# Optimization experiments

Hardware: AMD Instinct MI355X
Metric: run time of the kernel (lower is better)

Reference implementation:

```python
import jax, jax.numpy as jnp
import numpy as np

N_NODES = 10000
N_MOTIFS = 2500          # N_NODES / subgraph_size(=4)
N_AUG = N_NODES + N_MOTIFS
N_EDGES = 500000
NFEAT = 512
NHID = 128


def setup_inputs() -> dict:
    key = jax.random.key(0)
    ks = jax.random.split(key, 14)
    s = 0.05  # param init scale
    return {
        "x": jax.random.normal(ks[0], (N_NODES, NFEAT), jnp.float32),
        "edge_index": jax.random.randint(ks[1], (2, N_EDGES), 0, N_AUG, jnp.int64),
        "motif_list": jax.random.randint(ks[2], (N_MOTIFS, 4), 0, N_NODES, jnp.int64),
        "W1": jax.random.normal(ks[3], (NFEAT, 2 * NHID), jnp.float32) * s,
        "a_src1": jax.random.normal(ks[4], (2 * NHID,), jnp.float32) * s,
        "a_dst1": jax.random.normal(ks[5], (2 * NHID,), jnp.float32) * s,
        "b1": jnp.zeros((2 * NHID,), jnp.float32),
        "W2": jax.random.normal(ks[6], (2 * NHID, NHID), jnp.float32) * s,
        "a_src2": jax.random.normal(ks[7], (NHID,), jnp.float32) * s,
        "a_dst2": jax.random.normal(ks[8], (NHID,), jnp.float32) * s,
        "b2": jnp.zeros((NHID,), jnp.float32),
        "W_lin": jax.random.normal(ks[9], (NFEAT, NHID), jnp.float32) * s,  # torch Linear(nhid, nfeat) weight
        "b_lin": jnp.zeros((NFEAT,), jnp.float32),
    }


def gat_layer(x, src, dst, W, a_s, a_d, b, n):
    """Single-head GATConv (PyG semantics): edge-softmax attention over dst."""
    h = x @ W                                              # [n, out]
    alpha_s = h @ a_s                                      # [n]
    alpha_d = h @ a_d                                      # [n]
    e = jax.nn.leaky_relu(alpha_s[src] + alpha_d[dst], 0.2)  # [E]
    m = jax.ops.segment_max(e, dst, num_segments=n)        # stable softmax per dst
    w = jnp.exp(e - m[dst])
    denom = jax.ops.segment_sum(w, dst, num_segments=n)
    coef = w / (denom[dst] + 1e-16)                        # [E]
    out = jax.ops.segment_sum(coef[:, None] * h[src], dst, num_segments=n)
    return out + b


def reference(x, edge_index, motif_list, W1, a_src1, a_dst1, b1,
              W2, a_src2, a_dst2, b2, W_lin, b_lin):
    n = x.shape[0] + motif_list.shape[0]
    # augmented features: mean of each motif's node features appended as motif nodes
    x_aug = jnp.concatenate([x, jnp.mean(x[motif_list], axis=1)], axis=0)  # [N_AUG, F]
    # augmented edge list + self loops (GATConv adds self loops)
    loops = jnp.arange(n, dtype=edge_index.dtype)
    src = jnp.concatenate([edge_index[0], loops])
    dst = jnp.concatenate([edge_index[1], loops])
    h1 = gat_layer(x_aug, src, dst, W1, a_src1, a_dst1, b1, n)   # [N_AUG, 2*NHID]
    h2 = gat_layer(h1, src, dst, W2, a_src2, a_dst2, b2, n)      # [N_AUG, NHID]
    rec_adj = jax.nn.sigmoid(h2 @ h2.T)                          # [N_AUG, N_AUG]
    rec_feature = jax.nn.sigmoid(h2 @ W_lin.T + b_lin)           # [N_AUG, NFEAT]
    return (rec_feature, rec_adj)
```

## Files before the change

kernel.cpp:

```cpp
#include <hip/hip_runtime.h>

typedef unsigned short u16;
typedef unsigned int   u32;
typedef __attribute__((ext_vector_type(8))) short short8;
typedef __attribute__((ext_vector_type(4))) float f32x4;

#define N_NODES 10000
#define N_MOTIFS 2500
#define N_AUG   12500
#define N_EDGES 500000
#define E_TOT   512500
#define NFEAT   512
#define NH1     256
#define NH2     128

__device__ __forceinline__ float b2f(u16 u){ return __uint_as_float(((u32)u) << 16); }
__device__ __forceinline__ u16 f2b(float f){
  u32 x = __float_as_uint(f);
  x += 0x7fffu + ((x >> 16) & 1u);
  return (u16)(x >> 16);
}

#define PREP_Z   (N_AUG + 8)
#define PREP_W1  (NFEAT * NH1)
#define PREP_W2  (NH1 * NH2)
#define PREP_WL  (NFEAT * NH2)
#define PREP_TOT (PREP_Z + PREP_W1 + PREP_W2 + PREP_WL)

__global__ void k_prep(const float* __restrict__ W1, const float* __restrict__ W2,
                       const float* __restrict__ Wl, int* __restrict__ cnt,
                       u16* __restrict__ W1T, u16* __restrict__ W2T, u16* __restrict__ Wlb){
  int i = blockIdx.x * blockDim.x + threadIdx.x;
  if (i < PREP_Z){ cnt[i] = 0; return; }
  i -= PREP_Z;
  if (i < PREP_W1){
    int r = i / NH1, c = i - r * NH1;
    W1T[(size_t)c * NFEAT + r] = f2b(W1[i]);
    return;
  }
  i -= PREP_W1;
  if (i < PREP_W2){
    int r = i / NH2, c = i - r * NH2;
    W2T[(size_t)c * NH1 + r] = f2b(W2[i]);
    return;
  }
  i -= PREP_W2;
  if (i < PREP_WL) Wlb[i] = f2b(Wl[i]);
}

__global__ void k_xaug(const float* __restrict__ x, const int* __restrict__ motif,
                       u16* __restrict__ xb){
  int gid = blockIdx.x * blockDim.x + threadIdx.x;
  int row = gid >> 6;
  int c   = (gid & 63) << 3;
  if (row >= N_AUG) return;
  float v[8];
  if (row < N_NODES){
    const float* s = &x[(size_t)row * NFEAT + c];
    #pragma unroll
    for (int k = 0; k < 8; ++k) v[k] = s[k];
  } else {
    int m = row - N_NODES;
    const float* p0 = &x[(size_t)motif[m*4+0] * NFEAT + c];
    const float* p1 = &x[(size_t)motif[m*4+1] * NFEAT + c];
    const float* p2 = &x[(size_t)motif[m*4+2] * NFEAT + c];
    const float* p3 = &x[(size_t)motif[m*4+3] * NFEAT + c];
    #pragma unroll
    for (int k = 0; k < 8; ++k) v[k] = (p0[k] + p1[k] + p2[k] + p3[k]) * 0.25f;
  }
  short8 o;
  #pragma unroll
  for (int k = 0; k < 8; ++k) o[k] = (short)f2b(v[k]);
  *(short8*)&xb[(size_t)row * NFEAT + c] = o;
}

__global__ void k_hist(const int* __restrict__ ei, int* __restrict__ cnt){
  int i = blockIdx.x * blockDim.x + threadIdx.x;
  if (i >= E_TOT) return;
  int d = (i < N_EDGES) ? ei[N_EDGES + i] : (i - N_EDGES);
  atomicAdd(&cnt[d], 1);
}

__global__ void k_scan(const int* __restrict__ cnt, int* __restrict__ offs, int* __restrict__ cur){
  __shared__ int part[1024];
  int t = threadIdx.x;
  const int CH = 13;
  int base = t * CH;
  int s = 0;
  for (int i = 0; i < CH; ++i){ int idx = base + i; if (idx < N_AUG) s += cnt[idx]; }
  part[t] = s;
  __syncthreads();
  for (int off = 1; off < 1024; off <<= 1){
    int v = 0;
    if (t >= off) v = part[t - off];
    __syncthreads();
    if (t >= off) part[t] += v;
    __syncthreads();
  }
  int run = (t == 0) ? 0 : part[t - 1];
  for (int i = 0; i < CH; ++i){
    int idx = base + i;
    if (idx <= N_AUG){
      offs[idx] = run;
      if (idx < N_AUG){ cur[idx] = run; run += cnt[idx]; }
    }
  }
}

__global__ void k_scatter(const int* __restrict__ ei, int* __restrict__ cur, int* __restrict__ srcs){
  int i = blockIdx.x * blockDim.x + threadIdx.x;
  if (i >= E_TOT) return;
  int s, d;
  if (i < N_EDGES){ s = ei[i]; d = ei[N_EDGES + i]; } else { s = i - N_EDGES; d = s; }
  int pos = atomicAdd(&cur[d], 1);
  srcs[pos] = s;
}

template<int DIM>
__global__ void k_alpha(const u16* __restrict__ h, const float* __restrict__ avs,
                        const float* __restrict__ avd, float* __restrict__ oS, float* __restrict__ oD){
  __shared__ float shS[8], shD[8];
  int n = blockIdx.x, t = threadIdx.x;
  int lane = t & 63, wid = t >> 6;
  float hv = b2f(h[(size_t)n * DIM + t]);
  float s = hv * avs[t];
  float d = hv * avd[t];
  #pragma unroll
  for (int o = 32; o; o >>= 1){ s += __shfl_down(s, o); d += __shfl_down(d, o); }
  if (lane == 0){ shS[wid] = s; shD[wid] = d; }
  __syncthreads();
  if (t == 0){
    float ss = 0.f, dd = 0.f;
    #pragma unroll
    for (int i = 0; i < DIM/64; ++i){ ss += shS[i]; dd += shD[i]; }
    oS[n] = ss; oD[n] = dd;
  }
}

template<int DIM, int T>
__global__ __launch_bounds__(T) void k_agg(
    const int* __restrict__ offs, const int* __restrict__ srcs,
    const float* __restrict__ aS, const float* __restrict__ aD,
    const u16* __restrict__ hb, const float* __restrict__ bias,
    u16* __restrict__ hout){
  constexpr int NW = T / 64;
  __shared__ float rsh[2];
  __shared__ float wsh[128];
  __shared__ int   ssh[128];
  int d = blockIdx.x, t = threadIdx.x;
  int lane = t & 63, wid = t >> 6;
  int r0 = offs[d], r1 = offs[d + 1];
  float adv = aD[d];

  float mx = -3.0e38f;
  for (int j = r0 + t; j < r1; j += T){
    float e = aS[srcs[j]] + adv;
    e = (e >= 0.f) ? e : 0.2f * e;
    mx = fmaxf(mx, e);
  }
  #pragma unroll
  for (int o = 32; o; o >>= 1) mx = fmaxf(mx, __shfl_down(mx, o));
  if constexpr (NW == 2){
    if (lane == 0) rsh[wid] = mx;
    __syncthreads();
    mx = fmaxf(rsh[0], rsh[1]);
    __syncthreads();
  } else {
    mx = __shfl(mx, 0);
  }

  float sm = 0.f;
  for (int j = r0 + t; j < r1; j += T){
    float e = aS[srcs[j]] + adv;
    e = (e >= 0.f) ? e : 0.2f * e;
    sm += __expf(e - mx);
  }
  #pragma unroll
  for (int o = 32; o; o >>= 1) sm += __shfl_down(sm, o);
  if constexpr (NW == 2){
    if (lane == 0) rsh[wid] = sm;
    __syncthreads();
    sm = rsh[0] + rsh[1];
  } else {
    sm = __shfl(sm, 0);
  }

  float a0 = 0.f, a1 = 0.f;
  for (int base = r0; base < r1; base += 128){
    int cntE = min(128, r1 - base);
    __syncthreads();
    for (int j = t; j < cntE; j += T){
      int s = srcs[base + j];
      ssh[j] = s;
      float e = aS[s] + adv;
      e = (e >= 0.f) ? e : 0.2f * e;
      wsh[j] = __expf(e - mx);
    }
    __syncthreads();
    #pragma unroll 4
    for (int j = 0; j < cntE; ++j){
      u32 v = *(const u32*)&hb[(size_t)ssh[j] * DIM + 2*t];
      float w = wsh[j];
      a0 = fmaf(w, b2f((u16)(v & 0xffffu)), a0);
      a1 = fmaf(w, b2f((u16)(v >> 16)), a1);
    }
  }
  float inv = 1.f / (sm + 1e-16f);
  float o0 = a0 * inv + bias[2*t];
  float o1 = a1 * inv + bias[2*t + 1];
  u32 pv = (u32)f2b(o0) | ((u32)f2b(o1) << 16);
  *(u32*)&hout[(size_t)d * DIM + 2*t] = pv;
}

template<int EPI>
__global__ __launch_bounds__(256) void k_gemm(
    const u16* __restrict__ A, const u16* __restrict__ B,
    void* __restrict__ Cv, const float* __restrict__ bias,
    int M, int N, int K){
  __shared__ union SM {
    struct { u16 As[128][72]; u16 Bs[128][72]; } ab;
    float stage[64][132];
  } sm;
  int t = threadIdx.x;
  int lane = t & 63, wid = t >> 6;
  int wm = wid >> 1, wn = wid & 1;
  int m0 = blockIdx.y * 128, n0 = blockIdx.x * 128;

  f32x4 acc[4][4];
  #pragma unroll
  for (int i = 0; i < 4; ++i)
    #pragma unroll
    for (int j = 0; j < 4; ++j)
      acc[i][j] = {0.f, 0.f, 0.f, 0.f};

  for (int k0 = 0; k0 < K; k0 += 64){
    __syncthreads();
    #pragma unroll
    for (int i = 0; i < 4; ++i){
      int id = t + i * 256;
      int r = id >> 3, c = (id & 7) << 3;
      int gm = m0 + r; if (gm >= M) gm = M - 1;
      int gn = n0 + r; if (gn >= N) gn = N - 1;
      *(short8*)&sm.ab.As[r][c] = *(const short8*)&A[(size_t)gm * K + k0 + c];
      *(short8*)&sm.ab.Bs[r][c] = *(const short8*)&B[(size_t)gn * K + k0 + c];
    }
    __syncthreads();
    #pragma unroll
    for (int kk = 0; kk < 2; ++kk){
      int kof = kk * 32 + (lane >> 4) * 8;
      short8 af[4], bfr[4];
      #pragma unroll
      for (int mi = 0; mi < 4; ++mi) af[mi]  = *(const short8*)&sm.ab.As[wm*64 + mi*16 + (lane & 15)][kof];
      #pragma unroll
      for (int ni = 0; ni < 4; ++ni) bfr[ni] = *(const short8*)&sm.ab.Bs[wn*64 + ni*16 + (lane & 15)][kof];
      #pragma unroll
      for (int mi = 0; mi < 4; ++mi)
        #pragma unroll
        for (int ni = 0; ni < 4; ++ni)
          acc[mi][ni] = __builtin_amdgcn_mfma_f32_16x16x32_bf16(af[mi], bfr[ni], acc[mi][ni], 0, 0, 0);
    }
  }

  if (EPI == 0){
    u16* C = (u16*)Cv;
    #pragma unroll
    for (int mi = 0; mi < 4; ++mi)
      #pragma unroll
      for (int ni = 0; ni < 4; ++ni){
        int gn = n0 + wn*64 + ni*16 + (lane & 15);
        if (gn >= N) continue;
        #pragma unroll
        for (int r = 0; r < 4; ++r){
          int gm = m0 + wm*64 + mi*16 + (lane >> 4)*4 + r;
          if (gm >= M) continue;
          C[(size_t)gm * N + gn] = f2b(acc[mi][ni][r]);
        }
      }
  } else {
    float* C = (float*)Cv;
    #pragma unroll
    for (int half = 0; half < 2; ++half){
      __syncthreads();
      if (wm == half){
        #pragma unroll
        for (int mi = 0; mi < 4; ++mi)
          #pragma unroll
          for (int ni = 0; ni < 4; ++ni){
            int col = wn*64 + ni*16 + (lane & 15);
            int gn  = n0 + col;
            int gnc = (gn < N) ? gn : (N - 1);
            #pragma unroll
            for (int r = 0; r < 4; ++r){
              int lrow = mi*16 + (lane >> 4)*4 + r;
              float v = acc[mi][ni][r];
              if (EPI == 2) v += bias[gnc];
              v = 1.f / (1.f + __expf(-v));
              sm.stage[lrow][col] = v;
            }
          }
      }
      __syncthreads();
      #pragma unroll
      for (int pss = 0; pss < 8; ++pss){
        int flat = pss * 1024 + t * 4;
        int lr = flat >> 7, c = flat & 127;
        int gm = m0 + half*64 + lr;
        if (gm >= M) continue;
        int gn = n0 + c;
        f32x4 v = *(const f32x4*)&sm.stage[lr][c];
        if (gn + 3 < N){
          __builtin_nontemporal_store(v, (f32x4*)&C[(size_t)gm * N + gn]);
        } else {
          #pragma unroll
          for (int e = 0; e < 4; ++e)
            if (gn + e < N) C[(size_t)gm * N + gn + e] = v[e];
        }
      }
    }
  }
}

extern "C" void kernel_launch(void* const* d_in, const int* in_sizes, int n_in,
                              void* d_out, int out_size, void* d_ws, size_t ws_size,
                              hipStream_t stream){
  const float* x    = (const float*)d_in[0];
  const int*   ei   = (const int*)d_in[1];
  const int*   mot  = (const int*)d_in[2];
  const float* W1   = (const float*)d_in[3];
  const float* a_s1 = (const float*)d_in[4];
  const float* a_d1 = (const float*)d_in[5];
  const float* b1   = (const float*)d_in[6];
  const float* W2   = (const float*)d_in[7];
  const float* a_s2 = (const float*)d_in[8];
  const float* a_d2 = (const float*)d_in[9];
  const float* b2   = (const float*)d_in[10];
  const float* Wl   = (const float*)d_in[11];
  const float* bl   = (const float*)d_in[12];

  char* p = (char*)d_ws;
  auto alloc = [&](size_t bytes){ void* r = (void*)p; p += (bytes + 255) & ~(size_t)255; return r; };
  u16*   xaugb = (u16*)alloc((size_t)N_AUG * NFEAT * 2);
  u16*   W1T   = (u16*)alloc((size_t)NH1 * NFEAT * 2);
  u16*   W2T   = (u16*)alloc((size_t)NH2 * NH1 * 2);
  u16*   Wlb   = (u16*)alloc((size_t)NFEAT * NH2 * 2);
  u16*   h1b   = (u16*)alloc((size_t)N_AUG * NH1 * 2);
  u16*   h1out = (u16*)alloc((size_t)N_AUG * NH1 * 2);
  u16*   h2b   = (u16*)alloc((size_t)N_AUG * NH2 * 2);
  u16*   h2o   = (u16*)alloc((size_t)N_AUG * NH2 * 2);
  float* aS    = (float*)alloc((size_t)N_AUG * 4);
  float* aD    = (float*)alloc((size_t)N_AUG * 4);
  int*   cnt   = (int*)alloc((size_t)(N_AUG + 8) * 4);
  int*   offs  = (int*)alloc((size_t)(N_AUG + 8) * 4);
  int*   cur   = (int*)alloc((size_t)(N_AUG + 8) * 4);
  int*   srcs  = (int*)alloc((size_t)E_TOT * 4);

  float* out_feat = (float*)d_out;
  float* out_adj  = out_feat + (size_t)N_AUG * NFEAT;

  k_prep<<<(PREP_TOT + 255) / 256, 256, 0, stream>>>(W1, W2, Wl, cnt, W1T, W2T, Wlb);
  k_xaug<<<(N_AUG * 64 + 255) / 256, 256, 0, stream>>>(x, mot, xaugb);
  k_hist<<<(E_TOT + 255) / 256, 256, 0, stream>>>(ei, cnt);
  k_scan<<<1, 1024, 0, stream>>>(cnt, offs, cur);
  k_scatter<<<(E_TOT + 255) / 256, 256, 0, stream>>>(ei, cur, srcs);

  { dim3 g(NH1 / 128, 98); k_gemm<0><<<g, 256, 0, stream>>>(xaugb, W1T, h1b, nullptr, N_AUG, NH1, NFEAT); }
  k_alpha<NH1><<<N_AUG, NH1, 0, stream>>>(h1b, a_s1, a_d1, aS, aD);
  k_agg<NH1, 128><<<N_AUG, 128, 0, stream>>>(offs, srcs, aS, aD, h1b, b1, h1out);

  { dim3 g(1, 98); k_gemm<0><<<g, 256, 0, stream>>>(h1out, W2T, h2b, nullptr, N_AUG, NH2, NH1); }
  k_alpha<NH2><<<N_AUG, NH2, 0, stream>>>(h2b, a_s2, a_d2, aS, aD);
  k_agg<NH2, 64><<<N_AUG, 64, 0, stream>>>(offs, srcs, aS, aD, h2b, b2, h2o);

  { dim3 g(NFEAT / 128, 98); k_gemm<2><<<g, 256, 0, stream>>>(h2o, Wlb, out_feat, bl, N_AUG, NFEAT, NH2); }
  { dim3 g(98, 98);          k_gemm<1><<<g, 256, 0, stream>>>(h2o, h2o, out_adj, nullptr, N_AUG, N_AUG, NH2); }
}
```

Baseline: 434.0 us.

## Reassociate layer-1 aggregation with W2 and drop softmax max pass

Uses linearity to multiply h1 by W2 before the layer-1 edge aggregation, so the aggregation gathers 128-wide rows instead of 256-wide ones. The bias term becomes b1·W2, precomputed in the prep kernel. The aggregation kernel also drops the separate max and sum passes and computes unnormalized exp weights and their sum in a single pass. This removes two gather passes over edges but risks overflow in exp without max subtraction, and adds extra bf16 rounding from the reordered products.

```diff
diff --git a/kernel.cpp b/kernel.cpp
--- a/kernel.cpp
+++ b/kernel.cpp
@@ -25,11 +25,14 @@
 #define PREP_W1  (NFEAT * NH1)
 #define PREP_W2  (NH1 * NH2)
 #define PREP_WL  (NFEAT * NH2)
-#define PREP_TOT (PREP_Z + PREP_W1 + PREP_W2 + PREP_WL)
+#define PREP_B   (NH2)
+#define PREP_TOT (PREP_Z + PREP_W1 + PREP_W2 + PREP_WL + PREP_B)
 
 __global__ void k_prep(const float* __restrict__ W1, const float* __restrict__ W2,
-                       const float* __restrict__ Wl, int* __restrict__ cnt,
-                       u16* __restrict__ W1T, u16* __restrict__ W2T, u16* __restrict__ Wlb){
+                       const float* __restrict__ Wl, const float* __restrict__ b1,
+                       int* __restrict__ cnt,
+                       u16* __restrict__ W1T, u16* __restrict__ W2T, u16* __restrict__ Wlb,
+                       float* __restrict__ b1W2){
   int i = blockIdx.x * blockDim.x + threadIdx.x;
   if (i < PREP_Z){ cnt[i] = 0; return; }
   i -= PREP_Z;
@@ -45,7 +48,14 @@
     return;
   }
   i -= PREP_W2;
-  if (i < PREP_WL) Wlb[i] = f2b(Wl[i]);
+  if (i < PREP_WL){ Wlb[i] = f2b(Wl[i]); return; }
+  i -= PREP_WL;
+  if (i < PREP_B){
+    float s = 0.f;
+    #pragma unroll 8
+    for (int k = 0; k < NH1; ++k) s += b1[k] * W2[(size_t)k * NH2 + i];
+    b1W2[i] = s;
+  }
 }
 
 __global__ void k_xaug(const float* __restrict__ x, const int* __restrict__ motif,
@@ -137,79 +147,47 @@
   }
 }
 
-template<int DIM, int T>
-__global__ __launch_bounds__(T) void k_agg(
+__global__ __launch_bounds__(64) void k_agg128(
     const int* __restrict__ offs, const int* __restrict__ srcs,
     const float* __restrict__ aS, const float* __restrict__ aD,
     const u16* __restrict__ hb, const float* __restrict__ bias,
     u16* __restrict__ hout){
-  constexpr int NW = T / 64;
-  __shared__ float rsh[2];
   __shared__ float wsh[128];
   __shared__ int   ssh[128];
   int d = blockIdx.x, t = threadIdx.x;
-  int lane = t & 63, wid = t >> 6;
   int r0 = offs[d], r1 = offs[d + 1];
   float adv = aD[d];
 
-  float mx = -3.0e38f;
-  for (int j = r0 + t; j < r1; j += T){
-    float e = aS[srcs[j]] + adv;
-    e = (e >= 0.f) ? e : 0.2f * e;
-    mx = fmaxf(mx, e);
-  }
-  #pragma unroll
-  for (int o = 32; o; o >>= 1) mx = fmaxf(mx, __shfl_down(mx, o));
-  if constexpr (NW == 2){
-    if (lane == 0) rsh[wid] = mx;
-    __syncthreads();
-    mx = fmaxf(rsh[0], rsh[1]);
-    __syncthreads();
-  } else {
-    mx = __shfl(mx, 0);
-  }
-
-  float sm = 0.f;
-  for (int j = r0 + t; j < r1; j += T){
-    float e = aS[srcs[j]] + adv;
-    e = (e >= 0.f) ? e : 0.2f * e;
-    sm += __expf(e - mx);
-  }
-  #pragma unroll
-  for (int o = 32; o; o >>= 1) sm += __shfl_down(sm, o);
-  if constexpr (NW == 2){
-    if (lane == 0) rsh[wid] = sm;
-    __syncthreads();
-    sm = rsh[0] + rsh[1];
-  } else {
-    sm = __shfl(sm, 0);
-  }
-
-  float a0 = 0.f, a1 = 0.f;
+  float a0 = 0.f, a1 = 0.f, smp = 0.f;
   for (int base = r0; base < r1; base += 128){
     int cntE = min(128, r1 - base);
     __syncthreads();
-    for (int j = t; j < cntE; j += T){
+    for (int j = t; j < cntE; j += 64){
       int s = srcs[base + j];
       ssh[j] = s;
       float e = aS[s] + adv;
       e = (e >= 0.f) ? e : 0.2f * e;
-      wsh[j] = __expf(e - mx);
+      float w = __expf(e);
+      wsh[j] = w;
+      smp += w;
     }
     __syncthreads();
     #pragma unroll 4
     for (int j = 0; j < cntE; ++j){
-      u32 v = *(const u32*)&hb[(size_t)ssh[j] * DIM + 2*t];
+      u32 v = *(const u32*)&hb[(size_t)ssh[j] * NH2 + 2*t];
       float w = wsh[j];
       a0 = fmaf(w, b2f((u16)(v & 0xffffu)), a0);
       a1 = fmaf(w, b2f((u16)(v >> 16)), a1);
     }
   }
-  float inv = 1.f / (sm + 1e-16f);
+  #pragma unroll
+  for (int o = 32; o; o >>= 1) smp += __shfl_down(smp, o);
+  smp = __shfl(smp, 0);
+  float inv = 1.f / (smp + 1e-16f);
   float o0 = a0 * inv + bias[2*t];
   float o1 = a1 * inv + bias[2*t + 1];
   u32 pv = (u32)f2b(o0) | ((u32)f2b(o1) << 16);
-  *(u32*)&hout[(size_t)d * DIM + 2*t] = pv;
+  *(u32*)&hout[(size_t)d * NH2 + 2*t] = pv;
 }
 
 template<int EPI>
@@ -339,38 +317,39 @@
 
   char* p = (char*)d_ws;
   auto alloc = [&](size_t bytes){ void* r = (void*)p; p += (bytes + 255) & ~(size_t)255; return r; };
-  u16*   xaugb = (u16*)alloc((size_t)N_AUG * NFEAT * 2);
-  u16*   W1T   = (u16*)alloc((size_t)NH1 * NFEAT * 2);
-  u16*   W2T   = (u16*)alloc((size_t)NH2 * NH1 * 2);
-  u16*   Wlb   = (u16*)alloc((size_t)NFEAT * NH2 * 2);
-  u16*   h1b   = (u16*)alloc((size_t)N_AUG * NH1 * 2);
-  u16*   h1out = (u16*)alloc((size_t)N_AUG * NH1 * 2);
-  u16*   h2b   = (u16*)alloc((size_t)N_AUG * NH2 * 2);
-  u16*   h2o   = (u16*)alloc((size_t)N_AUG * NH2 * 2);
-  float* aS    = (float*)alloc((size_t)N_AUG * 4);
-  float* aD    = (float*)alloc((size_t)N_AUG * 4);
-  int*   cnt   = (int*)alloc((size_t)(N_AUG + 8) * 4);
-  int*   offs  = (int*)alloc((size_t)(N_AUG + 8) * 4);
-  int*   cur   = (int*)alloc((size_t)(N_AUG + 8) * 4);
-  int*   srcs  = (int*)alloc((size_t)E_TOT * 4);
+  u16*   xaugb  = (u16*)alloc((size_t)N_AUG * NFEAT * 2);
+  u16*   W1T    = (u16*)alloc((size_t)NH1 * NFEAT * 2);
+  u16*   W2T    = (u16*)alloc((size_t)NH2 * NH1 * 2);
+  u16*   Wlb    = (u16*)alloc((size_t)NFEAT * NH2 * 2);
+  u16*   h1b    = (u16*)alloc((size_t)N_AUG * NH1 * 2);
+  u16*   g      = (u16*)alloc((size_t)N_AUG * NH2 * 2);
+  u16*   h2preb = (u16*)alloc((size_t)N_AUG * NH2 * 2);
+  u16*   h2o    = (u16*)alloc((size_t)N_AUG * NH2 * 2);
+  float* aS     = (float*)alloc((size_t)N_AUG * 4);
+  float* aD     = (float*)alloc((size_t)N_AUG * 4);
+  float* b1W2   = (float*)alloc((size_t)NH2 * 4);
+  int*   cnt    = (int*)alloc((size_t)(N_AUG + 8) * 4);
+  int*   offs   = (int*)alloc((size_t)(N_AUG + 8) * 4);
+  int*   cur    = (int*)alloc((size_t)(N_AUG + 8) * 4);
+  int*   srcs   = (int*)alloc((size_t)E_TOT * 4);
 
   float* out_feat = (float*)d_out;
   float* out_adj  = out_feat + (size_t)N_AUG * NFEAT;
 
-  k_prep<<<(PREP_TOT + 255) / 256, 256, 0, stream>>>(W1, W2, Wl, cnt, W1T, W2T, Wlb);
+  k_prep<<<(PREP_TOT + 255) / 256, 256, 0, stream>>>(W1, W2, Wl, b1, cnt, W1T, W2T, Wlb, b1W2);
   k_xaug<<<(N_AUG * 64 + 255) / 256, 256, 0, stream>>>(x, mot, xaugb);
   k_hist<<<(E_TOT + 255) / 256, 256, 0, stream>>>(ei, cnt);
   k_scan<<<1, 1024, 0, stream>>>(cnt, offs, cur);
   k_scatter<<<(E_TOT + 255) / 256, 256, 0, stream>>>(ei, cur, srcs);
 
-  { dim3 g(NH1 / 128, 98); k_gemm<0><<<g, 256, 0, stream>>>(xaugb, W1T, h1b, nullptr, N_AUG, NH1, NFEAT); }
+  { dim3 gr(NH1 / 128, 98); k_gemm<0><<<gr, 256, 0, stream>>>(xaugb, W1T, h1b, nullptr, N_AUG, NH1, NFEAT); }
   k_alpha<NH1><<<N_AUG, NH1, 0, stream>>>(h1b, a_s1, a_d1, aS, aD);
-  k_agg<NH1, 128><<<N_AUG, 128, 0, stream>>>(offs, srcs, aS, aD, h1b, b1, h1out);
-
-  { dim3 g(1, 98); k_gemm<0><<<g, 256, 0, stream>>>(h1out, W2T, h2b, nullptr, N_AUG, NH2, NH1); }
-  k_alpha<NH2><<<N_AUG, NH2, 0, stream>>>(h2b, a_s2, a_d2, aS, aD);
-  k_agg<NH2, 64><<<N_AUG, 64, 0, stream>>>(offs, srcs, aS, aD, h2b, b2, h2o);
-
-  { dim3 g(NFEAT / 128, 98); k_gemm<2><<<g, 256, 0, stream>>>(h2o, Wlb, out_feat, bl, N_AUG, NFEAT, NH2); }
-  { dim3 g(98, 98);          k_gemm<1><<<g, 256, 0, stream>>>(h2o, h2o, out_adj, nullptr, N_AUG, N_AUG, NH2); }
-}
+  { dim3 gr(1, 98); k_gemm<0><<<gr, 256, 0, stream>>>(h1b, W2T, g, nullptr, N_AUG, NH2, NH1); }
+  k_agg128<<<N_AUG, 64, 0, stream>>>(offs, srcs, aS, aD, g, b1W2, h2preb);
+
+  k_alpha<NH2><<<N_AUG, NH2, 0, stream>>>(h2preb, a_s2, a_d2, aS, aD);
+  k_agg128<<<N_AUG, 64, 0, stream>>>(offs, srcs, aS, aD, h2preb, b2, h2o);
+
+  { dim3 gr(NFEAT / 128, 98); k_gemm<2><<<gr, 256, 0, stream>>>(h2o, Wlb, out_feat, bl, N_AUG, NFEAT, NH2); }
+  { dim3 gr(98, 98);          k_gemm<1><<<gr, 256, 0, stream>>>(h2o, h2o, out_adj, nullptr, N_AUG, N_AUG, NH2); }
+}
```

Result: no change. 432.2 us (-0.4%).
